# Optimization experiments

Measured on AMD Instinct MI355X. Metric: run time of the kernel, lower is better.

## Reference

```python
import jax, jax.numpy as jnp
import numpy as np

EPS = 1e-9
TEMP = 1.0
TOP_K = 2


def setup_inputs() -> dict:
    key = jax.random.key(0)
    k1, k2, k3, k4 = jax.random.split(key, 4)
    B, T, D, DC, E = 8, 4096, 1024, 512, 64
    din = D + DC
    inputs = jax.random.normal(k1, (B, T, D), dtype=jnp.float32)
    cond = jax.random.normal(k2, (B, T, DC), dtype=jnp.float32)
    # CondRouterMLP params (bias=False): Linear(din -> 2*din), GELU, Linear(2*din -> E)
    W1 = jax.random.normal(k3, (2 * din, din), dtype=jnp.float32) / np.sqrt(din).astype(np.float32)
    W2 = jax.random.normal(k4, (E, 2 * din), dtype=jnp.float32) / np.sqrt(2 * din).astype(np.float32)
    return {"inputs": inputs, "cond": cond, "W1": W1, "W2": W2}


def reference(inputs, cond, W1, W2):
    B, T, D = inputs.shape
    # concat hidden states with condition, flatten tokens
    x = jnp.concatenate([inputs, cond], axis=-1).reshape(-1, D + cond.shape[-1])  # [N, din]
    h = jax.nn.gelu(x @ W1.T, approximate=False)          # [N, 2*din] (torch nn.GELU = exact erf)
    logits = h @ W2.T                                     # [N, E]
    logits = (logits - logits.max(axis=-1, keepdims=True)) / TEMP
    probs = jax.nn.softmax(logits, axis=-1) + EPS
    probs = jnp.clip(probs, EPS, 1.0 - EPS)               # [N, E]
    # eval-mode top-k selection
    top_v, top_i = jax.lax.top_k(probs, TOP_K)            # [N, k]
    N, E = probs.shape
    rows = jnp.arange(N)[:, None]
    router_mask = jnp.zeros_like(probs).at[rows, top_i].set(1.0)
    router_probs = jnp.zeros_like(probs).at[rows, top_i].set(top_v)
    router_probs = router_probs / router_probs.sum(axis=-1, keepdims=True)  # normalize=True
    return (
        router_mask.reshape(B, T, E),
        top_i.reshape(B, T, TOP_K),
        router_probs.reshape(B, T, E),
        probs.reshape(B, T, E),
    )
```

## Files before the change

kernel.cpp:

```cpp
#include <hip/hip_runtime.h>
#include <cmath>

#define N_TOK 32768
#define D0    1024
#define DCC   512
#define DIN   1536
#define JD    3072
#define NE    64
#define BM    128
#define BJ    256
#define NJC   (JD/BJ)
#define NIT   48
#define NTH   512
#define HS    36
#define EPSV  1e-9f

typedef _Float16 half8 __attribute__((ext_vector_type(8)));
typedef float    f32x4 __attribute__((ext_vector_type(4)));

#define SZ_A  16384
#define SZ_B  32768
#define OFF_A 0
#define OFF_B 32768
#define LDS_TOTAL 98304
#define OFF_H    0
#define OFF_LRED 0
#define OFF_EPI  36864

#define W1N   ((size_t)JD*DIN)
#define W2N   ((size_t)NE*JD)
#define XTN   ((size_t)N_TOK*DIN)
#define XT_G  (256*192*128)
#define W1T_G (192*3072)
#define W2T_G (384*64)

__device__ __forceinline__ f32x4 mfma16(half8 a, half8 b, f32x4 c) {
    return __builtin_amdgcn_mfma_f32_16x16x32_f16(a, b, c, 0, 0, 0);
}

__device__ __forceinline__ void split8(const float4 v0, const float4 v1, half8& hh, half8& hl) {
    float f[8] = {v0.x, v0.y, v0.z, v0.w, v1.x, v1.y, v1.z, v1.w};
    #pragma unroll
    for (int i = 0; i < 8; ++i) {
        _Float16 h = (_Float16)f[i];
        hh[i] = h;
        hl[i] = (_Float16)(f[i] - (float)h);
    }
}

__device__ __forceinline__ void gload16(const void* g, void* l) {
    __builtin_amdgcn_global_load_lds(
        (const __attribute__((address_space(1))) unsigned int*)g,
        (__attribute__((address_space(3))) unsigned int*)l, 16, 0, 0);
}

__global__ void presplit_w1t(const float* __restrict__ W1,
                             _Float16* __restrict__ hi, _Float16* __restrict__ lo) {
    int g = blockIdx.x * blockDim.x + threadIdx.x;
    if (g >= W1T_G) return;
    const int j  = g % JD;
    const int ko = g / JD;
    const float* src = W1 + (size_t)j * DIN + ko * 8;
    float4 v0 = *(const float4*)src;
    float4 v1 = *(const float4*)(src + 4);
    half8 h, l;
    split8(v0, v1, h, l);
    *(half8*)(hi + (size_t)g * 8) = h;
    *(half8*)(lo + (size_t)g * 8) = l;
}

__global__ void presplit_w2t(const float* __restrict__ W2,
                             _Float16* __restrict__ hi, _Float16* __restrict__ lo) {
    int g = blockIdx.x * blockDim.x + threadIdx.x;
    if (g >= W2T_G) return;
    const int e  = g & 63;
    const int jo = g >> 6;
    const float* src = W2 + (size_t)e * JD + jo * 8;
    float4 v0 = *(const float4*)src;
    float4 v1 = *(const float4*)(src + 4);
    half8 h, l;
    split8(v0, v1, h, l);
    *(half8*)(hi + (size_t)g * 8) = h;
    *(half8*)(lo + (size_t)g * 8) = l;
}

__global__ void presplit_xt(const float* __restrict__ inp, const float* __restrict__ cnd,
                            _Float16* __restrict__ hi, _Float16* __restrict__ lo) {
    int g = blockIdx.x * blockDim.x + threadIdx.x;
    if (g >= XT_G) return;
    const int r    = g & 127;
    const int ko   = (g >> 7) % 192;
    const int tile = g / (192 * 128);
    const int token = tile * 128 + r;
    const float* src = (ko < 128) ? (inp + (size_t)token * D0 + ko * 8)
                                  : (cnd + (size_t)token * DCC + (ko - 128) * 8);
    float4 v0 = *(const float4*)src;
    float4 v1 = *(const float4*)(src + 4);
    half8 h, l;
    split8(v0, v1, h, l);
    *(half8*)(hi + (size_t)g * 8) = h;
    *(half8*)(lo + (size_t)g * 8) = l;
}

__global__ __launch_bounds__(NTH, 1)
void router_v16(const _Float16* __restrict__ Xh, const _Float16* __restrict__ Xl,
                const _Float16* __restrict__ W1h, const _Float16* __restrict__ W1l,
                const _Float16* __restrict__ W2h, const _Float16* __restrict__ W2l,
                float* __restrict__ out_mask, float* __restrict__ out_topi,
                float* __restrict__ out_rp, float* __restrict__ out_probs)
{
    __shared__ __align__(16) char smem[LDS_TOTAL];

    const int tid  = threadIdx.x;
    const int lane = tid & 63;
    const int w    = tid >> 6;
    const int tg   = w >> 2;
    const int jg   = w & 3;
    const int l15  = lane & 15;
    const int lg   = lane >> 4;
    const int blk  = blockIdx.x;
    const int t0   = blk * BM;

    const int spl = w >> 2;
    const int sko = w & 3;

    int aoff[4], boff[4];
    #pragma unroll
    for (int tf = 0; tf < 4; ++tf) aoff[tf] = (lg*128 + tg*64 + tf*16 + l15) * 16;
    #pragma unroll
    for (int jf = 0; jf < 4; ++jf) boff[jf] = (lg*256 + jg*64 + jf*16 + l15) * 16;

    const f32x4 vzero = {0.f, 0.f, 0.f, 0.f};
    f32x4 lacc[4] = {vzero, vzero, vzero, vzero};

    const _Float16* const Wbp = spl ? W1l : W1h;
    const _Float16* const Xbp = spl ? Xl  : Xh;
    const size_t xbase = (size_t)blk * 192 * 128;

    _Float16* const myHh = (_Float16*)(smem + OFF_H + w * 9216);
    _Float16* const myHl = myHh + 2304;

    for (int jc = 0; jc < NJC; ++jc) {
        f32x4 acc1[4][4];
        #pragma unroll
        for (int tf = 0; tf < 4; ++tf)
            #pragma unroll
            for (int jf = 0; jf < 4; ++jf) acc1[tf][jf] = vzero;

        {
            const _Float16* asrc = Xbp + (xbase + (size_t)(0 + sko) * 128) * 8;
            char* adst = smem + OFF_A + spl * 8192 + sko * 2048;
            gload16(asrc + (size_t)lane * 8, adst);
            gload16(asrc + (size_t)(64 + lane) * 8, adst + 1024);
            const _Float16* bsrc = Wbp + ((size_t)sko * JD + jc * BJ) * 8;
            char* bdst = smem + OFF_B + spl * 16384 + sko * 4096;
            #pragma unroll
            for (int q = 0; q < 4; ++q)
                gload16(bsrc + (size_t)(q * 64 + lane) * 8, bdst + q * 1024);
        }
        __syncthreads();

        for (int it = 0; it < NIT; ++it) {
            const int cur = it & 1, nxt = cur ^ 1;
            const bool more = (it + 1 < NIT);
            if (more) {
                const _Float16* asrc = Xbp + (xbase + (size_t)((it + 1) * 4 + sko) * 128) * 8;
                char* adst = smem + OFF_A + nxt * SZ_A + spl * 8192 + sko * 2048;
                gload16(asrc + (size_t)lane * 8, adst);
                gload16(asrc + (size_t)(64 + lane) * 8, adst + 1024);
                const _Float16* bsrc = Wbp +
                    ((size_t)((it + 1) * 4 + sko) * JD + jc * BJ) * 8;
                char* bdst = smem + OFF_B + nxt * SZ_B + spl * 16384 + sko * 4096;
                #pragma unroll
                for (int q = 0; q < 4; ++q)
                    gload16(bsrc + (size_t)(q * 64 + lane) * 8, bdst + q * 1024);
            }
            const char* ab = smem + OFF_A + cur * SZ_A;
            const char* bb = smem + OFF_B + cur * SZ_B;
            half8 ah[4], al[4], bh[4], bl[4];
            #pragma unroll
            for (int tf = 0; tf < 4; ++tf) {
                ah[tf] = *(const half8*)(ab + aoff[tf]);
                al[tf] = *(const half8*)(ab + 8192 + aoff[tf]);
            }
            #pragma unroll
            for (int jf = 0; jf < 4; ++jf) {
                bh[jf] = *(const half8*)(bb + boff[jf]);
                bl[jf] = *(const half8*)(bb + 16384 + boff[jf]);
            }
            #pragma unroll
            for (int tf = 0; tf < 4; ++tf)
                #pragma unroll
                for (int jf = 0; jf < 4; ++jf) {
                    acc1[tf][jf] = mfma16(ah[tf], bh[jf], acc1[tf][jf]);
                    acc1[tf][jf] = mfma16(ah[tf], bl[jf], acc1[tf][jf]);
                    acc1[tf][jf] = mfma16(al[tf], bh[jf], acc1[tf][jf]);
                }
            __syncthreads();
        }

        #pragma unroll
        for (int r = 0; r < 2; ++r) {
            #pragma unroll
            for (int c = 0; c < 2; ++c) {
                const int jf = 2*r + c;
                #pragma unroll
                for (int tf = 0; tf < 4; ++tf)
                    #pragma unroll
                    for (int rr = 0; rr < 4; ++rr) {
                        const float v = acc1[tf][jf][rr];
                        const float gv = 0.5f * v * (1.0f + erff(v * 0.70710678118654752f));
                        const _Float16 gh = (_Float16)gv;
                        const _Float16 gl = (_Float16)(gv - (float)gh);
                        const int o = (tf*16 + lg*4 + rr) * HS + c*16 + l15;
                        myHh[o] = gh; myHl[o] = gl;
                    }
            }
            __syncthreads();
            #pragma unroll
            for (int s = 0; s < 4; ++s) {
                const _Float16* sh = (const _Float16*)(smem + OFF_H + (tg*4 + s) * 9216);
                const _Float16* sl = sh + 2304;
                const int jo = jc*32 + s*8 + r*4 + lg;
                const size_t wg = ((size_t)jo * 64 + jg*16 + l15) * 8;
                half8 b2h = *(const half8*)(W2h + wg);
                half8 b2l = *(const half8*)(W2l + wg);
                #pragma unroll
                for (int tf = 0; tf < 4; ++tf) {
                    const int o = (tf*16 + l15) * HS + lg*8;
                    half8 a2h = *(const half8*)(sh + o);
                    half8 a2l = *(const half8*)(sl + o);
                    lacc[tf] = mfma16(a2h, b2h, lacc[tf]);
                    lacc[tf] = mfma16(a2h, b2l, lacc[tf]);
                    lacc[tf] = mfma16(a2l, b2h, lacc[tf]);
                }
            }
            __syncthreads();
        }
    }

    float* const Lred = (float*)(smem + OFF_LRED);
    #pragma unroll
    for (int tf = 0; tf < 4; ++tf)
        #pragma unroll
        for (int rr = 0; rr < 4; ++rr)
            Lred[(tg*64 + tf*16 + lg*4 + rr) * 68 + jg*16 + l15] = lacc[tf][rr];
    __syncthreads();

    float* const mA   = (float*)(smem + OFF_EPI);
    float* const invA = mA + BM;
    int*   const i1A  = (int*)(invA + BM);
    int*   const i2A  = i1A + BM;
    float* const rp1A = (float*)(i2A + BM);
    float* const rp2A = rp1A + BM;

    if (tid < BM) {
        const float* row = Lred + tid * 68;
        float m = -3.402823466e38f;
        for (int e = 0; e < NE; ++e) m = fmaxf(m, row[e]);
        float s = 0.f, v1 = -3.402823466e38f, v2 = -3.402823466e38f;
        int i1 = 0, i2 = 0;
        for (int e = 0; e < NE; ++e) {
            const float v = row[e];
            s += expf(v - m);
            if (v > v1)      { v2 = v1; i2 = i1; v1 = v; i1 = e; }
            else if (v > v2) { v2 = v; i2 = e; }
        }
        const float inv = 1.f / s;
        const float p1 = fminf(expf(v1 - m) * inv + EPSV, 1.f - EPSV);
        const float p2 = fminf(expf(v2 - m) * inv + EPSV, 1.f - EPSV);
        mA[tid] = m; invA[tid] = inv; i1A[tid] = i1; i2A[tid] = i2;
        const float den = p1 + p2;
        rp1A[tid] = p1 / den; rp2A[tid] = p2 / den;
    }
    __syncthreads();

    for (int idx = tid; idx < BM * NE; idx += NTH) {
        const int r = idx >> 6, e = idx & 63;
        const size_t o = (size_t)(t0 + r) * NE + e;
        const float p = fminf(expf(Lred[r * 68 + e] - mA[r]) * invA[r] + EPSV, 1.f - EPSV);
        const int b1 = (e == i1A[r]), b2 = (e == i2A[r]);
        out_probs[o] = p;
        out_mask[o]  = (b1 | b2) ? 1.f : 0.f;
        out_rp[o]    = b1 ? rp1A[r] : (b2 ? rp2A[r] : 0.f);
    }
    if (tid < BM * 2) {
        const int r = tid >> 1, q = tid & 1;
        out_topi[(size_t)(t0 + r) * 2 + q] = (float)(q ? i2A[r] : i1A[r]);
    }
}

__global__ __launch_bounds__(NTH, 1)
void router_v9fb(const float* __restrict__ inp, const float* __restrict__ cnd,
                 const _Float16* __restrict__ W1h, const _Float16* __restrict__ W1l,
                 const _Float16* __restrict__ W2h, const _Float16* __restrict__ W2l,
                 float* __restrict__ out_mask, float* __restrict__ out_topi,
                 float* __restrict__ out_rp, float* __restrict__ out_probs)
{
    __shared__ __align__(16) char smem[LDS_TOTAL];
    const int tid  = threadIdx.x;
    const int lane = tid & 63;
    const int w    = tid >> 6;
    const int tg   = w >> 2;
    const int jg   = w & 3;
    const int l15  = lane & 15;
    const int lg   = lane >> 4;
    const int t0   = blockIdx.x * BM;
    const int akoct = w >> 1;
    const int arow  = (w & 1) * 64 + lane;
    const int bplane = w >> 2;
    const int bkoct  = w & 3;

    int aoff[4], boff[4];
    #pragma unroll
    for (int tf = 0; tf < 4; ++tf) aoff[tf] = (lg*128 + tg*64 + tf*16 + l15) * 16;
    #pragma unroll
    for (int jf = 0; jf < 4; ++jf) boff[jf] = (lg*256 + jg*64 + jf*16 + l15) * 16;

    const f32x4 vzero = {0.f, 0.f, 0.f, 0.f};
    f32x4 lacc[4] = {vzero, vzero, vzero, vzero};
    const float* const xrowA = inp + (size_t)(t0 + arow) * D0;
    const float* const xrowC = cnd + (size_t)(t0 + arow) * DCC;
    const _Float16* const Wbp = bplane ? W1l : W1h;
    _Float16* const myHh = (_Float16*)(smem + w * 9216);
    _Float16* const myHl = myHh + 2304;

    for (int jc = 0; jc < NJC; ++jc) {
        f32x4 acc1[4][4];
        #pragma unroll
        for (int tf = 0; tf < 4; ++tf)
            #pragma unroll
            for (int jf = 0; jf < 4; ++jf) acc1[tf][jf] = vzero;
        {
            #pragma unroll
            for (int q = 0; q < 4; ++q) {
                const _Float16* src = Wbp + ((size_t)bkoct * JD + jc*BJ + q*64 + lane) * 8;
                gload16(src, smem + OFF_B + bplane*16384 + bkoct*4096 + q*1024);
            }
            const float* sx = xrowA + akoct * 8;
            float4 v0 = *(const float4*)sx;
            float4 v1 = *(const float4*)(sx + 4);
            half8 hh, hl;
            split8(v0, v1, hh, hl);
            const int g = (akoct*128 + arow) * 16;
            *(half8*)(smem + g) = hh;
            *(half8*)(smem + 8192 + g) = hl;
        }
        __syncthreads();
        for (int it = 0; it < NIT; ++it) {
            const int cur = it & 1, nxt = cur ^ 1;
            const bool more = (it + 1 < NIT);
            float4 xv0, xv1;
            if (more) {
                const int ko = (it + 1) * 4 + bkoct;
                #pragma unroll
                for (int q = 0; q < 4; ++q) {
                    const _Float16* src = Wbp + ((size_t)ko * JD + jc*BJ + q*64 + lane) * 8;
                    gload16(src, smem + OFF_B + nxt*SZ_B + bplane*16384 + bkoct*4096 + q*1024);
                }
                const int k = (it + 1) * 32 + akoct * 8;
                const float* sx = (k < D0) ? (xrowA + k) : (xrowC + k - D0);
                xv0 = *(const float4*)sx;
                xv1 = *(const float4*)(sx + 4);
            }
            const char* ab = smem + cur*SZ_A;
            const char* bb = smem + OFF_B + cur*SZ_B;
            half8 ah[4], al[4], bh[4], bl[4];
            #pragma unroll
            for (int tf = 0; tf < 4; ++tf) {
                ah[tf] = *(const half8*)(ab + aoff[tf]);
                al[tf] = *(const half8*)(ab + 8192 + aoff[tf]);
            }
            #pragma unroll
            for (int jf = 0; jf < 4; ++jf) {
                bh[jf] = *(const half8*)(bb + boff[jf]);
                bl[jf] = *(const half8*)(bb + 16384 + boff[jf]);
            }
            #pragma unroll
            for (int tf = 0; tf < 4; ++tf)
                #pragma unroll
                for (int jf = 0; jf < 4; ++jf) {
                    acc1[tf][jf] = mfma16(ah[tf], bh[jf], acc1[tf][jf]);
                    acc1[tf][jf] = mfma16(ah[tf], bl[jf], acc1[tf][jf]);
                    acc1[tf][jf] = mfma16(al[tf], bh[jf], acc1[tf][jf]);
                }
            if (more) {
                half8 hh, hl;
                split8(xv0, xv1, hh, hl);
                const int g = (akoct*128 + arow) * 16;
                *(half8*)(smem + nxt*SZ_A + g) = hh;
                *(half8*)(smem + nxt*SZ_A + 8192 + g) = hl;
            }
            __syncthreads();
        }
        #pragma unroll
        for (int r = 0; r < 2; ++r) {
            #pragma unroll
            for (int c = 0; c < 2; ++c) {
                const int jf = 2*r + c;
                #pragma unroll
                for (int tf = 0; tf < 4; ++tf)
                    #pragma unroll
                    for (int rr = 0; rr < 4; ++rr) {
                        const float v = acc1[tf][jf][rr];
                        const float gv = 0.5f * v * (1.0f + erff(v * 0.70710678118654752f));
                        const _Float16 gh = (_Float16)gv;
                        const _Float16 gl = (_Float16)(gv - (float)gh);
                        const int o = (tf*16 + lg*4 + rr) * HS + c*16 + l15;
                        myHh[o] = gh; myHl[o] = gl;
                    }
            }
            __syncthreads();
            #pragma unroll
            for (int s = 0; s < 4; ++s) {
                const _Float16* sh = (const _Float16*)(smem + (tg*4 + s) * 9216);
                const _Float16* sl = sh + 2304;
                const int jo = jc*32 + s*8 + r*4 + lg;
                const size_t wg = ((size_t)jo * 64 + jg*16 + l15) * 8;
                half8 b2h = *(const half8*)(W2h + wg);
                half8 b2l = *(const half8*)(W2l + wg);
                #pragma unroll
                for (int tf = 0; tf < 4; ++tf) {
                    const int o = (tf*16 + l15) * HS + lg*8;
                    half8 a2h = *(const half8*)(sh + o);
                    half8 a2l = *(const half8*)(sl + o);
                    lacc[tf] = mfma16(a2h, b2h, lacc[tf]);
                    lacc[tf] = mfma16(a2h, b2l, lacc[tf]);
                    lacc[tf] = mfma16(a2l, b2h, lacc[tf]);
                }
            }
            __syncthreads();
        }
    }
    float* const Lred = (float*)(smem + OFF_LRED);
    #pragma unroll
    for (int tf = 0; tf < 4; ++tf)
        #pragma unroll
        for (int rr = 0; rr < 4; ++rr)
            Lred[(tg*64 + tf*16 + lg*4 + rr) * 68 + jg*16 + l15] = lacc[tf][rr];
    __syncthreads();
    float* const mA   = (float*)(smem + OFF_EPI);
    float* const invA = mA + BM;
    int*   const i1A  = (int*)(invA + BM);
    int*   const i2A  = i1A + BM;
    float* const rp1A = (float*)(i2A + BM);
    float* const rp2A = rp1A + BM;
    if (tid < BM) {
        const float* row = Lred + tid * 68;
        float m = -3.402823466e38f;
        for (int e = 0; e < NE; ++e) m = fmaxf(m, row[e]);
        float s = 0.f, v1 = -3.402823466e38f, v2 = -3.402823466e38f;
        int i1 = 0, i2 = 0;
        for (int e = 0; e < NE; ++e) {
            const float v = row[e];
            s += expf(v - m);
            if (v > v1)      { v2 = v1; i2 = i1; v1 = v; i1 = e; }
            else if (v > v2) { v2 = v; i2 = e; }
        }
        const float inv = 1.f / s;
        const float p1 = fminf(expf(v1 - m) * inv + EPSV, 1.f - EPSV);
        const float p2 = fminf(expf(v2 - m) * inv + EPSV, 1.f - EPSV);
        mA[tid] = m; invA[tid] = inv; i1A[tid] = i1; i2A[tid] = i2;
        const float den = p1 + p2;
        rp1A[tid] = p1 / den; rp2A[tid] = p2 / den;
    }
    __syncthreads();
    for (int idx = tid; idx < BM * NE; idx += NTH) {
        const int r = idx >> 6, e = idx & 63;
        const size_t o = (size_t)(t0 + r) * NE + e;
        const float p = fminf(expf(Lred[r * 68 + e] - mA[r]) * invA[r] + EPSV, 1.f - EPSV);
        const int b1 = (e == i1A[r]), b2 = (e == i2A[r]);
        out_probs[o] = p;
        out_mask[o]  = (b1 | b2) ? 1.f : 0.f;
        out_rp[o]    = b1 ? rp1A[r] : (b2 ? rp2A[r] : 0.f);
    }
    if (tid < BM * 2) {
        const int r = tid >> 1, q = tid & 1;
        out_topi[(size_t)(t0 + r) * 2 + q] = (float)(q ? i2A[r] : i1A[r]);
    }
}

extern "C" void kernel_launch(void* const* d_in, const int* in_sizes, int n_in,
                              void* d_out, int out_size, void* d_ws, size_t ws_size,
                              hipStream_t stream) {
    const float* inp = (const float*)d_in[0];
    const float* cnd = (const float*)d_in[1];
    const float* W1  = (const float*)d_in[2];
    const float* W2  = (const float*)d_in[3];

    float* out = (float*)d_out;
    const size_t NT = (size_t)N_TOK;
    float* out_mask  = out;
    float* out_topi  = out + NT * NE;
    float* out_rp    = out + NT * NE + NT * 2;
    float* out_probs = out + NT * NE + NT * 2 + NT * NE;

    const size_t V16_REQ = (2*XTN + 2*W1N + 2*W2N) * 2;
    if (ws_size >= V16_REQ) {
        _Float16* Xh  = (_Float16*)d_ws;
        _Float16* Xl  = Xh + XTN;
        _Float16* W1h = Xl + XTN;
        _Float16* W1l = W1h + W1N;
        _Float16* W2h = W1l + W1N;
        _Float16* W2l = W2h + W2N;
        hipLaunchKernelGGL(presplit_xt,  dim3(XT_G/256), dim3(256), 0, stream, inp, cnd, Xh, Xl);
        hipLaunchKernelGGL(presplit_w1t, dim3((W1T_G + 255)/256), dim3(256), 0, stream, W1, W1h, W1l);
        hipLaunchKernelGGL(presplit_w2t, dim3((W2T_G + 255)/256), dim3(256), 0, stream, W2, W2h, W2l);
        hipLaunchKernelGGL(router_v16, dim3(N_TOK / BM), dim3(NTH), 0, stream,
                           Xh, Xl, W1h, W1l, W2h, W2l,
                           out_mask, out_topi, out_rp, out_probs);
    } else {
        _Float16* W1h = (_Float16*)d_ws;
        _Float16* W1l = W1h + W1N;
        _Float16* W2h = W1l + W1N;
        _Float16* W2l = W2h + W2N;
        hipLaunchKernelGGL(presplit_w1t, dim3((W1T_G + 255)/256), dim3(256), 0, stream, W1, W1h, W1l);
        hipLaunchKernelGGL(presplit_w2t, dim3((W2T_G + 255)/256), dim3(256), 0, stream, W2, W2h, W2l);
        hipLaunchKernelGGL(router_v9fb, dim3(N_TOK / BM), dim3(NTH), 0, stream,
                           inp, cnd, W1h, W1l, W2h, W2l,
                           out_mask, out_topi, out_rp, out_probs);
    }
}
```

Baseline: 1.147 ms.

## Double the W1 column chunk per block to halve A-tile reloads

Widens the hidden-dimension chunk from 256 to 512 columns, so each warp computes a 4x8 fragment grid and the X tile is reloaded half as often per token block. LDS grows to 160 KB to hold the double-buffered wider B tiles, and the logits reduction and epilogue scratch are moved past the H staging area. The inner loop now loads B fragments one at a time and interleaves them with MFMAs to limit register pressure, though the accumulators double to 128 floats per lane. The fallback kernel keeps its old constants. Risks include register spills and longer GELU/second-GEMM phases per chunk.

After: 1.025 ms, median of 2. 10.6% less time.

```diff
diff --git a/kernel.cpp b/kernel.cpp
--- a/kernel.cpp
+++ b/kernel.cpp
@@ -8,7 +8,7 @@
 #define JD    3072
 #define NE    64
 #define BM    128
-#define BJ    256
+#define BJ    512
 #define NJC   (JD/BJ)
 #define NIT   48
 #define NTH   512
@@ -19,13 +19,13 @@
 typedef float    f32x4 __attribute__((ext_vector_type(4)));
 
 #define SZ_A  16384
-#define SZ_B  32768
+#define SZ_B  65536
 #define OFF_A 0
 #define OFF_B 32768
-#define LDS_TOTAL 98304
+#define LDS_TOTAL 163840
 #define OFF_H    0
-#define OFF_LRED 0
-#define OFF_EPI  36864
+#define OFF_LRED 73728
+#define OFF_EPI  (73728 + 34816)
 
 #define W1N   ((size_t)JD*DIN)
 #define W2N   ((size_t)NE*JD)
@@ -103,7 +103,7 @@
 }
 
 __global__ __launch_bounds__(NTH, 1)
-void router_v16(const _Float16* __restrict__ Xh, const _Float16* __restrict__ Xl,
+void router_v17(const _Float16* __restrict__ Xh, const _Float16* __restrict__ Xl,
                 const _Float16* __restrict__ W1h, const _Float16* __restrict__ W1l,
                 const _Float16* __restrict__ W2h, const _Float16* __restrict__ W2l,
                 float* __restrict__ out_mask, float* __restrict__ out_topi,
@@ -124,11 +124,11 @@
     const int spl = w >> 2;
     const int sko = w & 3;
 
-    int aoff[4], boff[4];
+    int aoff[4], boff[8];
     #pragma unroll
     for (int tf = 0; tf < 4; ++tf) aoff[tf] = (lg*128 + tg*64 + tf*16 + l15) * 16;
     #pragma unroll
-    for (int jf = 0; jf < 4; ++jf) boff[jf] = (lg*256 + jg*64 + jf*16 + l15) * 16;
+    for (int jf = 0; jf < 8; ++jf) boff[jf] = lg*8192 + (jg*128 + jf*16 + l15) * 16;
 
     const f32x4 vzero = {0.f, 0.f, 0.f, 0.f};
     f32x4 lacc[4] = {vzero, vzero, vzero, vzero};
@@ -141,21 +141,21 @@
     _Float16* const myHl = myHh + 2304;
 
     for (int jc = 0; jc < NJC; ++jc) {
-        f32x4 acc1[4][4];
+        f32x4 acc1[4][8];
         #pragma unroll
         for (int tf = 0; tf < 4; ++tf)
             #pragma unroll
-            for (int jf = 0; jf < 4; ++jf) acc1[tf][jf] = vzero;
+            for (int jf = 0; jf < 8; ++jf) acc1[tf][jf] = vzero;
 
         {
-            const _Float16* asrc = Xbp + (xbase + (size_t)(0 + sko) * 128) * 8;
+            const _Float16* asrc = Xbp + (xbase + (size_t)sko * 128) * 8;
             char* adst = smem + OFF_A + spl * 8192 + sko * 2048;
             gload16(asrc + (size_t)lane * 8, adst);
             gload16(asrc + (size_t)(64 + lane) * 8, adst + 1024);
             const _Float16* bsrc = Wbp + ((size_t)sko * JD + jc * BJ) * 8;
-            char* bdst = smem + OFF_B + spl * 16384 + sko * 4096;
-            #pragma unroll
-            for (int q = 0; q < 4; ++q)
+            char* bdst = smem + OFF_B + spl * 32768 + sko * 8192;
+            #pragma unroll
+            for (int q = 0; q < 8; ++q)
                 gload16(bsrc + (size_t)(q * 64 + lane) * 8, bdst + q * 1024);
         }
         __syncthreads();
@@ -170,37 +170,35 @@
                 gload16(asrc + (size_t)(64 + lane) * 8, adst + 1024);
                 const _Float16* bsrc = Wbp +
                     ((size_t)((it + 1) * 4 + sko) * JD + jc * BJ) * 8;
-                char* bdst = smem + OFF_B + nxt * SZ_B + spl * 16384 + sko * 4096;
-                #pragma unroll
-                for (int q = 0; q < 4; ++q)
+                char* bdst = smem + OFF_B + nxt * SZ_B + spl * 32768 + sko * 8192;
+                #pragma unroll
+                for (int q = 0; q < 8; ++q)
                     gload16(bsrc + (size_t)(q * 64 + lane) * 8, bdst + q * 1024);
             }
             const char* ab = smem + OFF_A + cur * SZ_A;
             const char* bb = smem + OFF_B + cur * SZ_B;
-            half8 ah[4], al[4], bh[4], bl[4];
+            half8 ah[4], al[4];
             #pragma unroll
             for (int tf = 0; tf < 4; ++tf) {
                 ah[tf] = *(const half8*)(ab + aoff[tf]);
                 al[tf] = *(const half8*)(ab + 8192 + aoff[tf]);
             }
             #pragma unroll
-            for (int jf = 0; jf < 4; ++jf) {
-                bh[jf] = *(const half8*)(bb + boff[jf]);
-                bl[jf] = *(const half8*)(bb + 16384 + boff[jf]);
-            }
-            #pragma unroll
-            for (int tf = 0; tf < 4; ++tf)
-                #pragma unroll
-                for (int jf = 0; jf < 4; ++jf) {
-                    acc1[tf][jf] = mfma16(ah[tf], bh[jf], acc1[tf][jf]);
-                    acc1[tf][jf] = mfma16(ah[tf], bl[jf], acc1[tf][jf]);
-                    acc1[tf][jf] = mfma16(al[tf], bh[jf], acc1[tf][jf]);
+            for (int jf = 0; jf < 8; ++jf) {
+                half8 bh = *(const half8*)(bb + boff[jf]);
+                half8 bl = *(const half8*)(bb + 32768 + boff[jf]);
+                #pragma unroll
+                for (int tf = 0; tf < 4; ++tf) {
+                    acc1[tf][jf] = mfma16(ah[tf], bh, acc1[tf][jf]);
+                    acc1[tf][jf] = mfma16(ah[tf], bl, acc1[tf][jf]);
+                    acc1[tf][jf] = mfma16(al[tf], bh, acc1[tf][jf]);
                 }
+            }
             __syncthreads();
         }
 
         #pragma unroll
-        for (int r = 0; r < 2; ++r) {
+        for (int r = 0; r < 4; ++r) {
             #pragma unroll
             for (int c = 0; c < 2; ++c) {
                 const int jf = 2*r + c;
@@ -221,7 +219,7 @@
             for (int s = 0; s < 4; ++s) {
                 const _Float16* sh = (const _Float16*)(smem + OFF_H + (tg*4 + s) * 9216);
                 const _Float16* sl = sh + 2304;
-                const int jo = jc*32 + s*8 + r*4 + lg;
+                const int jo = jc*64 + s*16 + r*4 + lg;
                 const size_t wg = ((size_t)jo * 64 + jg*16 + l15) * 8;
                 half8 b2h = *(const half8*)(W2h + wg);
                 half8 b2l = *(const half8*)(W2l + wg);
@@ -290,6 +288,11 @@
     }
 }
 
+#define FB_SZ_A  16384
+#define FB_SZ_B  32768
+#define FB_OFF_B 32768
+#define FB_LDS   98304
+
 __global__ __launch_bounds__(NTH, 1)
 void router_v9fb(const float* __restrict__ inp, const float* __restrict__ cnd,
                  const _Float16* __restrict__ W1h, const _Float16* __restrict__ W1l,
@@ -297,7 +300,7 @@
                  float* __restrict__ out_mask, float* __restrict__ out_topi,
                  float* __restrict__ out_rp, float* __restrict__ out_probs)
 {
-    __shared__ __align__(16) char smem[LDS_TOTAL];
+    __shared__ __align__(16) char smem[FB_LDS];
     const int tid  = threadIdx.x;
     const int lane = tid & 63;
     const int w    = tid >> 6;
@@ -325,7 +328,7 @@
     _Float16* const myHh = (_Float16*)(smem + w * 9216);
     _Float16* const myHl = myHh + 2304;
 
-    for (int jc = 0; jc < NJC; ++jc) {
+    for (int jc = 0; jc < JD/256; ++jc) {
         f32x4 acc1[4][4];
         #pragma unroll
         for (int tf = 0; tf < 4; ++tf)
@@ -334,8 +337,8 @@
         {
             #pragma unroll
             for (int q = 0; q < 4; ++q) {
-                const _Float16* src = Wbp + ((size_t)bkoct * JD + jc*BJ + q*64 + lane) * 8;
-                gload16(src, smem + OFF_B + bplane*16384 + bkoct*4096 + q*1024);
+                const _Float16* src = Wbp + ((size_t)bkoct * JD + jc*256 + q*64 + lane) * 8;
+                gload16(src, smem + FB_OFF_B + bplane*16384 + bkoct*4096 + q*1024);
             }
             const float* sx = xrowA + akoct * 8;
             float4 v0 = *(const float4*)sx;
@@ -355,16 +358,16 @@
                 const int ko = (it + 1) * 4 + bkoct;
                 #pragma unroll
                 for (int q = 0; q < 4; ++q) {
-                    const _Float16* src = Wbp + ((size_t)ko * JD + jc*BJ + q*64 + lane) * 8;
-                    gload16(src, smem + OFF_B + nxt*SZ_B + bplane*16384 + bkoct*4096 + q*1024);
+                    const _Float16* src = Wbp + ((size_t)ko * JD + jc*256 + q*64 + lane) * 8;
+                    gload16(src, smem + FB_OFF_B + nxt*FB_SZ_B + bplane*16384 + bkoct*4096 + q*1024);
                 }
                 const int k = (it + 1) * 32 + akoct * 8;
                 const float* sx = (k < D0) ? (xrowA + k) : (xrowC + k - D0);
                 xv0 = *(const float4*)sx;
                 xv1 = *(const float4*)(sx + 4);
             }
-            const char* ab = smem + cur*SZ_A;
-            const char* bb = smem + OFF_B + cur*SZ_B;
+            const char* ab = smem + cur*FB_SZ_A;
+            const char* bb = smem + FB_OFF_B + cur*FB_SZ_B;
             half8 ah[4], al[4], bh[4], bl[4];
             #pragma unroll
             for (int tf = 0; tf < 4; ++tf) {
@@ -388,8 +391,8 @@
                 half8 hh, hl;
                 split8(xv0, xv1, hh, hl);
                 const int g = (akoct*128 + arow) * 16;
-                *(half8*)(smem + nxt*SZ_A + g) = hh;
-                *(half8*)(smem + nxt*SZ_A + 8192 + g) = hl;
+                *(half8*)(smem + nxt*FB_SZ_A + g) = hh;
+                *(half8*)(smem + nxt*FB_SZ_A + 8192 + g) = hl;
             }
             __syncthreads();
         }
@@ -432,14 +435,14 @@
             __syncthreads();
         }
     }
-    float* const Lred = (float*)(smem + OFF_LRED);
+    float* const Lred = (float*)smem;
     #pragma unroll
     for (int tf = 0; tf < 4; ++tf)
         #pragma unroll
         for (int rr = 0; rr < 4; ++rr)
             Lred[(tg*64 + tf*16 + lg*4 + rr) * 68 + jg*16 + l15] = lacc[tf][rr];
     __syncthreads();
-    float* const mA   = (float*)(smem + OFF_EPI);
+    float* const mA   = (float*)(smem + 36864);
     float* const invA = mA + BM;
     int*   const i1A  = (int*)(invA + BM);
     int*   const i2A  = i1A + BM;
@@ -495,8 +498,8 @@
     float* out_rp    = out + NT * NE + NT * 2;
     float* out_probs = out + NT * NE + NT * 2 + NT * NE;
 
-    const size_t V16_REQ = (2*XTN + 2*W1N + 2*W2N) * 2;
-    if (ws_size >= V16_REQ) {
+    const size_t V17_REQ = (2*XTN + 2*W1N + 2*W2N) * 2;
+    if (ws_size >= V17_REQ) {
         _Float16* Xh  = (_Float16*)d_ws;
         _Float16* Xl  = Xh + XTN;
         _Float16* W1h = Xl + XTN;
@@ -506,7 +509,7 @@
         hipLaunchKernelGGL(presplit_xt,  dim3(XT_G/256), dim3(256), 0, stream, inp, cnd, Xh, Xl);
         hipLaunchKernelGGL(presplit_w1t, dim3((W1T_G + 255)/256), dim3(256), 0, stream, W1, W1h, W1l);
         hipLaunchKernelGGL(presplit_w2t, dim3((W2T_G + 255)/256), dim3(256), 0, stream, W2, W2h, W2l);
-        hipLaunchKernelGGL(router_v16, dim3(N_TOK / BM), dim3(NTH), 0, stream,
+        hipLaunchKernelGGL(router_v17, dim3(N_TOK / BM), dim3(NTH), 0, stream,
                            Xh, Xl, W1h, W1l, W2h, W2l,
                            out_mask, out_topi, out_rp, out_probs);
     } else {
```
